# Optimization experiments

Hardware: AMD Instinct MI355X
Metric: run time of the kernel (lower is better)

## Reference

```python
import jax, jax.numpy as jnp
import numpy as np

DIM = 1024
NUM_HEADS = 16
HEAD_DIM = DIM // NUM_HEADS


def _rope_tables(seq_len, dim, dtype):
    # matches llama_rotary_embedding: inv_freq over even indices of head_dim
    inv_freq = 1.0 / (10000.0 ** (jnp.arange(0, dim, 2, dtype=jnp.float32) / dim))
    t = jnp.arange(seq_len, dtype=jnp.float32)
    freqs = jnp.outer(t, inv_freq)  # [S, dim/2]
    return jnp.cos(freqs).astype(dtype), jnp.sin(freqs).astype(dtype)


def _apply_rope(x, cos_emb, sin_emb):
    # x: [B, H, S, hd]; takes interleaved halves, concatenates rotated halves
    x1 = x[..., 0::2]
    x2 = x[..., 1::2]
    return jnp.concatenate((x1 * cos_emb - x2 * sin_emb,
                            x1 * sin_emb + x2 * cos_emb), axis=-1)


def setup_inputs() -> dict:
    key = jax.random.key(0)
    k_x, k_qkv, k_out, k_b = jax.random.split(key, 4)
    B, S, D = 2, 2048, DIM
    x = jax.random.normal(k_x, (B, S, D), dtype=jnp.float32)
    # torch nn.Linear weights are [out_features, in_features]
    w_qkv = jax.random.normal(k_qkv, (3 * D, D), dtype=jnp.float32) * (1.0 / np.sqrt(D))
    w_out = jax.random.normal(k_out, (D, D), dtype=jnp.float32) * (1.0 / np.sqrt(D))
    b_out = jax.random.normal(k_b, (D,), dtype=jnp.float32) * 0.01
    return {"x": x, "w_qkv": w_qkv, "w_out": w_out, "b_out": b_out}


def reference(x, w_qkv, w_out, b_out):
    B, S, D = x.shape
    H, hd = NUM_HEADS, HEAD_DIM
    qkv = jnp.einsum('bsd,ed->bse', x, w_qkv)  # [B, S, 3D]
    q, k, v = jnp.split(qkv, 3, axis=-1)
    # [B, S, D] -> [B, H, S, hd]
    q, k, v = (t.reshape(B, S, H, hd).transpose(0, 2, 1, 3) for t in (q, k, v))
    cos_emb, sin_emb = _rope_tables(S, hd, x.dtype)  # [S, hd/2]
    q = _apply_rope(q, cos_emb, sin_emb)
    k = _apply_rope(k, cos_emb, sin_emb)
    scores = jnp.einsum('bhqd,bhkd->bhqk', q, k) / jnp.sqrt(jnp.asarray(hd, x.dtype))
    attn = jax.nn.softmax(scores, axis=-1)
    out = jnp.einsum('bhqk,bhkd->bhqd', attn, v)
    out = out.transpose(0, 2, 1, 3).reshape(B, S, D)
    return jnp.einsum('bsd,ed->bse', out, w_out) + b_out
```

## Files before the change

### kernel.cpp

```cpp
#include <hip/hip_runtime.h>
#include <math.h>

typedef __bf16 bf16_t;
typedef bf16_t bf16x8 __attribute__((ext_vector_type(8)));
typedef bf16_t bf16x4 __attribute__((ext_vector_type(4)));
typedef short  s16x4  __attribute__((ext_vector_type(4)));
typedef float  f32x4  __attribute__((ext_vector_type(4)));

#define DIM_   1024
#define NHEADS 16
#define HDIM   64
#define SEQ    2048
#define BATCH  2

#define QK_SCALE 0.18033688011112042f

__device__ __forceinline__ s16x4 as_s16x4(bf16x4 v) {
    union { bf16x4 b; s16x4 s; } u; u.b = v; return u.s;
}

__device__ __forceinline__ void gld16(const bf16_t* g, bf16_t* l) {
    __builtin_amdgcn_global_load_lds(
        (const __attribute__((address_space(1))) void*)g,
        (__attribute__((address_space(3))) void*)l, 16, 0, 0);
}

#define XCNT   (4096u * 1024u)
#define WQCNT  (3072u * 1024u)
#define WOCNT  (1024u * 1024u)
__global__ __launch_bounds__(256) void cast3(const float* __restrict__ s0,
                                             const float* __restrict__ s1,
                                             const float* __restrict__ s2,
                                             bf16_t* __restrict__ d0,
                                             bf16_t* __restrict__ d1,
                                             bf16_t* __restrict__ d2) {
    size_t i = ((size_t)blockIdx.x * 256 + threadIdx.x) * 8;
    const float* s; bf16_t* d; size_t off;
    if (i < XCNT)               { s = s0; d = d0; off = i; }
    else if (i < XCNT + WQCNT)  { s = s1; d = d1; off = i - XCNT; }
    else                        { s = s2; d = d2; off = i - XCNT - WQCNT; }
    float4 a = *(const float4*)(s + off);
    float4 b = *(const float4*)(s + off + 4);
    bf16x8 o = { (bf16_t)a.x, (bf16_t)a.y, (bf16_t)a.z, (bf16_t)a.w,
                 (bf16_t)b.x, (bf16_t)b.y, (bf16_t)b.z, (bf16_t)b.w };
    *(bf16x8*)(d + off) = o;
}

template <bool QKV>
__global__ __launch_bounds__(256) void gemm_lds(const bf16_t* __restrict__ A,
                                                const bf16_t* __restrict__ B,
                                                const float* __restrict__ bias,
                                                void* __restrict__ Cout,
                                                bf16_t* __restrict__ vt,
                                                int M, int N, int K) {
    __shared__ __align__(16) bf16_t As[128 * 32];
    __shared__ __align__(16) bf16_t Bs[128 * 32];
    const int tid  = threadIdx.x;
    const int m0   = blockIdx.y * 128;
    const int n0   = blockIdx.x * 128;
    const int w    = tid >> 6;
    const int lane = tid & 63;
    const int m16  = lane & 15;
    const int quad = lane >> 4;
    const int wm   = (w >> 1) * 64;
    const int wn   = (w & 1) * 64;
    const int lrow = lane >> 2;
    const int lcol = (lane & 3) * 8;

    const bf16_t* pa0 = A + (size_t)(m0 + w * 16 + lrow) * K + lcol;
    const bf16_t* pb0 = B + (size_t)(n0 + w * 16 + lrow) * K + lcol;
    bf16_t* lA0 = &As[(w * 16) * 32];
    bf16_t* lA1 = &As[(64 + w * 16) * 32];
    bf16_t* lB0 = &Bs[(w * 16) * 32];
    bf16_t* lB1 = &Bs[(64 + w * 16) * 32];

    f32x4 acc[4][4] = {};

    for (int k0 = 0; k0 < K; k0 += 32) {
        __syncthreads();
        gld16(pa0 + k0, lA0);
        gld16(pa0 + (size_t)64 * K + k0, lA1);
        gld16(pb0 + k0, lB0);
        gld16(pb0 + (size_t)64 * K + k0, lB1);
        __syncthreads();

        bf16x8 af[4], bfr[4];
#pragma unroll
        for (int i = 0; i < 4; ++i)
            af[i] = *(const bf16x8*)(&As[(wm + i * 16 + m16) * 32 + quad * 8]);
#pragma unroll
        for (int j = 0; j < 4; ++j)
            bfr[j] = *(const bf16x8*)(&Bs[(wn + j * 16 + m16) * 32 + quad * 8]);
#pragma unroll
        for (int i = 0; i < 4; ++i)
#pragma unroll
            for (int j = 0; j < 4; ++j)
                acc[i][j] = __builtin_amdgcn_mfma_f32_16x16x32_bf16(af[i], bfr[j], acc[i][j], 0, 0, 0);
    }

    if (QKV && n0 >= 2 * DIM_) {
        const int b      = m0 >> 11;
        const int s_base = (m0 & (SEQ - 1)) + wm;
#pragma unroll
        for (int j = 0; j < 4; ++j) {
            const int cit = wn + j * 16 + m16;
            const int h   = ((n0 - 2 * DIM_) >> 6) + (cit >> 6);
            const int d   = cit & 63;
            bf16_t* vrow = vt + ((size_t)(b * 16 + h) * 64 + d) * SEQ + s_base;
#pragma unroll
            for (int i = 0; i < 4; ++i) {
                bf16x4 ov = { (bf16_t)acc[i][j][0], (bf16_t)acc[i][j][1],
                              (bf16_t)acc[i][j][2], (bf16_t)acc[i][j][3] };
                *(bf16x4*)(vrow + i * 16 + quad * 4) = ov;
            }
        }
    } else if (QKV) {
        bf16_t* C = (bf16_t*)Cout;
#pragma unroll
        for (int i = 0; i < 4; ++i)
#pragma unroll
            for (int j = 0; j < 4; ++j) {
                const int col = n0 + wn + j * 16 + m16;
#pragma unroll
                for (int r = 0; r < 4; ++r)
                    C[(size_t)(m0 + wm + i * 16 + quad * 4 + r) * N + col] = (bf16_t)acc[i][j][r];
            }
    } else {
        float* C = (float*)Cout;
#pragma unroll
        for (int j = 0; j < 4; ++j) {
            const int col = n0 + wn + j * 16 + m16;
            const float bv = bias[col];
#pragma unroll
            for (int i = 0; i < 4; ++i)
#pragma unroll
                for (int r = 0; r < 4; ++r)
                    C[(size_t)(m0 + wm + i * 16 + quad * 4 + r) * N + col] = acc[i][j][r] + bv;
        }
    }
}

__global__ __launch_bounds__(256) void gemm_out64(const bf16_t* __restrict__ A,
                                                  const bf16_t* __restrict__ B,
                                                  const float* __restrict__ bias,
                                                  float* __restrict__ C,
                                                  int M, int N, int K) {
    __shared__ __align__(16) bf16_t As[128 * 32];
    __shared__ __align__(16) bf16_t Bs[64 * 32];
    const int tid  = threadIdx.x;
    const int m0   = blockIdx.y * 128;
    const int n0   = blockIdx.x * 64;
    const int w    = tid >> 6;
    const int lane = tid & 63;
    const int m16  = lane & 15;
    const int quad = lane >> 4;
    const int wm   = (w >> 1) * 64;
    const int wn   = (w & 1) * 32;
    const int lrow = lane >> 2;
    const int lcol = (lane & 3) * 8;

    const bf16_t* pa0 = A + (size_t)(m0 + w * 16 + lrow) * K + lcol;
    const bf16_t* pb0 = B + (size_t)(n0 + w * 16 + lrow) * K + lcol;
    bf16_t* lA0 = &As[(w * 16) * 32];
    bf16_t* lA1 = &As[(64 + w * 16) * 32];
    bf16_t* lB0 = &Bs[(w * 16) * 32];

    f32x4 acc[4][2] = {};

    for (int k0 = 0; k0 < K; k0 += 32) {
        __syncthreads();
        gld16(pa0 + k0, lA0);
        gld16(pa0 + (size_t)64 * K + k0, lA1);
        gld16(pb0 + k0, lB0);
        __syncthreads();

        bf16x8 af[4], bfr[2];
#pragma unroll
        for (int i = 0; i < 4; ++i)
            af[i] = *(const bf16x8*)(&As[(wm + i * 16 + m16) * 32 + quad * 8]);
#pragma unroll
        for (int j = 0; j < 2; ++j)
            bfr[j] = *(const bf16x8*)(&Bs[(wn + j * 16 + m16) * 32 + quad * 8]);
#pragma unroll
        for (int i = 0; i < 4; ++i)
#pragma unroll
            for (int j = 0; j < 2; ++j)
                acc[i][j] = __builtin_amdgcn_mfma_f32_16x16x32_bf16(af[i], bfr[j], acc[i][j], 0, 0, 0);
    }

#pragma unroll
    for (int j = 0; j < 2; ++j) {
        const int col = n0 + wn + j * 16 + m16;
        const float bv = bias[col];
#pragma unroll
        for (int i = 0; i < 4; ++i)
#pragma unroll
            for (int r = 0; r < 4; ++r)
                C[(size_t)(m0 + wm + i * 16 + quad * 4 + r) * N + col] = acc[i][j][r] + bv;
    }
}

__global__ __launch_bounds__(256) void rope_bf16(bf16_t* __restrict__ qkv) {
    __shared__ float ctab[8][32];
    __shared__ float stab[8][32];
    const int tid = threadIdx.x;
    const int sl  = tid >> 5, j = tid & 31;
    const int s   = (int)((blockIdx.x * 8 + sl) & (SEQ - 1));
    const float freq = exp2f(-0.41524101186092029f * (float)j);
    float sn, cs;
    sincosf((float)s * freq, &sn, &cs);
    ctab[sl][j] = cs;
    stab[sl][j] = sn;
    __syncthreads();

    const int gid   = blockIdx.x * 256 + tid;
    const int m     = gid >> 5;
    const int rr    = gid & 31;
    const int which = rr >> 4;
    const int hh    = rr & 15;
    const float osc = (which == 0) ? QK_SCALE : 1.0f;

    bf16_t* p = qkv + (size_t)m * (3 * DIM_) + which * DIM_ + hh * HDIM;
    union { bf16_t e[64]; bf16x8 v[8]; } X, O;
#pragma unroll
    for (int i = 0; i < 8; ++i) X.v[i] = *(const bf16x8*)(p + i * 8);
#pragma unroll
    for (int t = 0; t < 32; ++t) {
        const float x1 = (float)X.e[2 * t];
        const float x2 = (float)X.e[2 * t + 1];
        const float c  = ctab[sl][t];
        const float s2 = stab[sl][t];
        O.e[t]      = (bf16_t)((x1 * c - x2 * s2) * osc);
        O.e[32 + t] = (bf16_t)((x1 * s2 + x2 * c) * osc);
    }
#pragma unroll
    for (int i = 0; i < 8; ++i) *(bf16x8*)(p + i * 8) = O.v[i];
}

__global__ __launch_bounds__(256) void attn_mfma(const bf16_t* __restrict__ qkv,
                                                 const bf16_t* __restrict__ vt,
                                                 bf16_t* __restrict__ out) {
    __shared__ __align__(16) char smem[37888];
    bf16_t* Ks0  = (bf16_t*)smem;
    bf16_t* Vt0  = (bf16_t*)(smem + 9216);
    bf16_t* Ks1  = (bf16_t*)(smem + 18432);
    bf16_t* Vt1  = (bf16_t*)(smem + 27648);
    float*  Ored = (float*)smem;
    float*  Lred = (float*)(smem + 36864);

    const int tid  = threadIdx.x;
    const int w    = tid >> 6;
    const int lane = tid & 63;
    const int m16  = lane & 15;
    const int quad = lane >> 4;
    const int bh   = blockIdx.y;
    const int b    = bh >> 4;
    const int hh   = bh & 15;
    const int q0   = blockIdx.x * 64;

    const size_t rs = 3 * DIM_;
    const bf16_t* qbase = qkv + (size_t)(b * SEQ) * rs + hh * HDIM;
    const bf16_t* kbase = qbase + DIM_;
    const bf16_t* vtg   = vt + (size_t)bh * 64 * SEQ;

    bf16x8 qf[4][2];
#pragma unroll
    for (int n = 0; n < 4; ++n)
#pragma unroll
        for (int kt = 0; kt < 2; ++kt)
            qf[n][kt] = *(const bf16x8*)(qbase + (size_t)(q0 + n * 16 + m16) * rs + kt * 32 + quad * 8);

    f32x4 o[4][4] = {};
    float lp[4] = {};

    const int srow = tid >> 3;
    const int sc8  = (tid & 7) * 8;

    bf16x8 kreg[2], vreg[2];

#pragma unroll
    for (int p = 0; p < 2; ++p) {
        const int row = srow + p * 32;
        kreg[p] = *(const bf16x8*)(kbase + (size_t)row * rs + sc8);
        vreg[p] = *(const bf16x8*)(vtg + (size_t)row * SEQ + sc8);
    }
#pragma unroll
    for (int p = 0; p < 2; ++p) {
        const int row = srow + p * 32;
        *(bf16x8*)(&Ks0[row * 72 + sc8]) = kreg[p];
        *(bf16x8*)(&Vt0[row * 72 + sc8]) = vreg[p];
    }
    __syncthreads();

    const bf16_t* kg0 = kbase + (size_t)(64 + srow) * rs + sc8;
    const bf16_t* kg1 = kg0 + (size_t)32 * rs;
    const bf16_t* vg0 = vtg + (size_t)srow * SEQ + 64 + sc8;
    const bf16_t* vg1 = vg0 + (size_t)32 * SEQ;
    const size_t kadv = (size_t)64 * rs;

#define ATTN_BODY(T, KS, VS, KSN, VSN)                                             \
    do {                                                                           \
        const int tt = (T);                                                        \
        if (tt < 31) {                                                             \
            kreg[0] = *(const bf16x8*)(kg0);                                       \
            kreg[1] = *(const bf16x8*)(kg1);                                       \
            vreg[0] = *(const bf16x8*)(vg0);                                       \
            vreg[1] = *(const bf16x8*)(vg1);                                       \
            kg0 += kadv; kg1 += kadv; vg0 += 64; vg1 += 64;                        \
        }                                                                          \
        bf16x8 ak0 = *(const bf16x8*)(&KS[(w * 16 + m16) * 72 + 0 * 32 + quad * 8]); \
        bf16x8 ak1 = *(const bf16x8*)(&KS[(w * 16 + m16) * 72 + 1 * 32 + quad * 8]); \
        bf16x4 va[4];                                                              \
        _Pragma("unroll")                                                          \
        for (int ds = 0; ds < 4; ++ds)                                             \
            va[ds] = *(const bf16x4*)(&VS[(ds * 16 + m16) * 72 + w * 16 + quad * 4]); \
        s16x4 pb[4];                                                               \
        _Pragma("unroll")                                                          \
        for (int n = 0; n < 4; ++n) {                                              \
            f32x4 c = {};                                                          \
            c = __builtin_amdgcn_mfma_f32_16x16x32_bf16(ak0, qf[n][0], c, 0, 0, 0); \
            c = __builtin_amdgcn_mfma_f32_16x16x32_bf16(ak1, qf[n][1], c, 0, 0, 0); \
            bf16x4 pv;                                                             \
            _Pragma("unroll")                                                      \
            for (int r = 0; r < 4; ++r) {                                          \
                const float pp = __builtin_amdgcn_exp2f(c[r]);                     \
                lp[n] += pp;                                                       \
                pv[r] = (bf16_t)pp;                                                \
            }                                                                      \
            pb[n] = as_s16x4(pv);                                                  \
        }                                                                          \
        __builtin_amdgcn_s_setprio(1);                                             \
        _Pragma("unroll")                                                          \
        for (int ds = 0; ds < 4; ++ds)                                             \
            _Pragma("unroll")                                                      \
            for (int n = 0; n < 4; ++n)                                            \
                o[ds][n] = __builtin_amdgcn_mfma_f32_16x16x16bf16_1k(               \
                    as_s16x4(va[ds]), pb[n], o[ds][n], 0, 0, 0);                   \
        __builtin_amdgcn_s_setprio(0);                                             \
        if (tt < 31) {                                                             \
            _Pragma("unroll")                                                      \
            for (int p = 0; p < 2; ++p) {                                          \
                const int row = srow + p * 32;                                     \
                *(bf16x8*)(&KSN[row * 72 + sc8]) = kreg[p];                        \
                *(bf16x8*)(&VSN[row * 72 + sc8]) = vreg[p];                        \
            }                                                                      \
        }                                                                          \
        __syncthreads();                                                           \
    } while (0)

    for (int t = 0; t < 32; t += 2) {
        ATTN_BODY(t,     Ks0, Vt0, Ks1, Vt1);
        ATTN_BODY(t + 1, Ks1, Vt1, Ks0, Vt0);
    }
#undef ATTN_BODY

#pragma unroll
    for (int n = 0; n < 4; ++n) {
        lp[n] += __shfl_xor(lp[n], 16);
        lp[n] += __shfl_xor(lp[n], 32);
    }
    if (quad == 0) {
#pragma unroll
        for (int n = 0; n < 4; ++n) Lred[w * 64 + n * 16 + m16] = lp[n];
    }
    __syncthreads();
    const float linv = 1.0f / (Lred[lane] + Lred[64 + lane] + Lred[128 + lane] + Lred[192 + lane]);

    const size_t obase = (size_t)(b * SEQ + q0 + lane) * DIM_ + hh * HDIM;
#pragma unroll
    for (int p = 0; p < 4; ++p) {
        __syncthreads();
#pragma unroll
        for (int n = 0; n < 4; ++n)
#pragma unroll
            for (int r = 0; r < 4; ++r)
                Ored[w * 1040 + (quad * 4 + r) * 65 + n * 16 + m16] = o[p][n][r];
        __syncthreads();
        union { bf16_t e[4]; bf16x4 v; } ob;
#pragma unroll
        for (int d = 0; d < 4; ++d) {
            const int dd = w * 4 + d;
            const float v = Ored[dd * 65 + lane] + Ored[1040 + dd * 65 + lane] +
                            Ored[2080 + dd * 65 + lane] + Ored[3120 + dd * 65 + lane];
            ob.e[d] = (bf16_t)(v * linv);
        }
        *(bf16x4*)(out + obase + p * 16 + w * 4) = ob.v;
    }
}

extern "C" void kernel_launch(void* const* d_in, const int* in_sizes, int n_in,
                              void* d_out, int out_size, void* d_ws, size_t ws_size,
                              hipStream_t stream) {
    const float* x     = (const float*)d_in[0];
    const float* w_qkv = (const float*)d_in[1];
    const float* w_out = (const float*)d_in[2];
    const float* b_out = (const float*)d_in[3];
    float* out = (float*)d_out;

    const int M = BATCH * SEQ;

    bf16_t* qkv_b  = (bf16_t*)d_ws;
    bf16_t* attn_b = qkv_b + (size_t)M * 3 * DIM_;
    bf16_t* vt_b   = attn_b + (size_t)M * DIM_;
    bf16_t* xb     = vt_b + (size_t)BATCH * NHEADS * HDIM * SEQ;
    bf16_t* wqkvb  = xb + (size_t)M * DIM_;
    bf16_t* woutb  = wqkvb + (size_t)3 * DIM_ * DIM_;

    cast3<<<(XCNT + WQCNT + WOCNT) / (256 * 8), 256, 0, stream>>>(
        x, w_qkv, w_out, xb, wqkvb, woutb);

    gemm_lds<true><<<dim3(3 * DIM_ / 128, M / 128), 256, 0, stream>>>(
        xb, wqkvb, nullptr, qkv_b, vt_b, M, 3 * DIM_, DIM_);

    rope_bf16<<<(M * 2 * NHEADS) / 256, 256, 0, stream>>>(qkv_b);

    attn_mfma<<<dim3(SEQ / 64, BATCH * NHEADS), 256, 0, stream>>>(qkv_b, vt_b, attn_b);

    gemm_out64<<<dim3(DIM_ / 64, M / 128), 256, 0, stream>>>(
        attn_b, woutb, b_out, out, M, DIM_, DIM_);
}
```

Baseline: 213.4 us.

## Double-buffer LDS tiles in both GEMM kernels to overlap loads with MFMA

Both GEMM kernels now keep two LDS buffers per operand. Each iteration issues global_load_lds for the next K-tile into the alternate buffer before running MFMAs on the current one, so the per-iteration barrier count drops from two to one. The intent is to hide global-to-LDS latency behind compute. The cost is twice the LDS footprint, which may lower occupancy. Correctness relies on the compiler inserting the right vmcnt waits before the barrier, since the async LDS writes must complete before the next iteration reads them.

```diff
diff --git a/kernel.cpp b/kernel.cpp
--- a/kernel.cpp
+++ b/kernel.cpp
@@ -53,8 +53,8 @@
                                                 void* __restrict__ Cout,
                                                 bf16_t* __restrict__ vt,
                                                 int M, int N, int K) {
-    __shared__ __align__(16) bf16_t As[128 * 32];
-    __shared__ __align__(16) bf16_t Bs[128 * 32];
+    __shared__ __align__(16) bf16_t As[2][128 * 32];
+    __shared__ __align__(16) bf16_t Bs[2][128 * 32];
     const int tid  = threadIdx.x;
     const int m0   = blockIdx.y * 128;
     const int n0   = blockIdx.x * 128;
@@ -69,33 +69,42 @@
 
     const bf16_t* pa0 = A + (size_t)(m0 + w * 16 + lrow) * K + lcol;
     const bf16_t* pb0 = B + (size_t)(n0 + w * 16 + lrow) * K + lcol;
-    bf16_t* lA0 = &As[(w * 16) * 32];
-    bf16_t* lA1 = &As[(64 + w * 16) * 32];
-    bf16_t* lB0 = &Bs[(w * 16) * 32];
-    bf16_t* lB1 = &Bs[(64 + w * 16) * 32];
+    const int sOffA0 = (w * 16) * 32;
+    const int sOffA1 = (64 + w * 16) * 32;
+
+    gld16(pa0, (bf16_t*)As + sOffA0);
+    gld16(pa0 + (size_t)64 * K, (bf16_t*)As + sOffA1);
+    gld16(pb0, (bf16_t*)Bs + sOffA0);
+    gld16(pb0 + (size_t)64 * K, (bf16_t*)Bs + sOffA1);
+    __syncthreads();
 
     f32x4 acc[4][4] = {};
+    int buf = 0;
 
     for (int k0 = 0; k0 < K; k0 += 32) {
-        __syncthreads();
-        gld16(pa0 + k0, lA0);
-        gld16(pa0 + (size_t)64 * K + k0, lA1);
-        gld16(pb0 + k0, lB0);
-        gld16(pb0 + (size_t)64 * K + k0, lB1);
-        __syncthreads();
-
+        const int nb = buf ^ 1;
+        if (k0 + 32 < K) {
+            gld16(pa0 + k0 + 32, (bf16_t*)As + nb * 4096 + sOffA0);
+            gld16(pa0 + (size_t)64 * K + k0 + 32, (bf16_t*)As + nb * 4096 + sOffA1);
+            gld16(pb0 + k0 + 32, (bf16_t*)Bs + nb * 4096 + sOffA0);
+            gld16(pb0 + (size_t)64 * K + k0 + 32, (bf16_t*)Bs + nb * 4096 + sOffA1);
+        }
+        const bf16_t* sA = (const bf16_t*)As + buf * 4096;
+        const bf16_t* sB = (const bf16_t*)Bs + buf * 4096;
         bf16x8 af[4], bfr[4];
 #pragma unroll
         for (int i = 0; i < 4; ++i)
-            af[i] = *(const bf16x8*)(&As[(wm + i * 16 + m16) * 32 + quad * 8]);
+            af[i] = *(const bf16x8*)(sA + (wm + i * 16 + m16) * 32 + quad * 8);
 #pragma unroll
         for (int j = 0; j < 4; ++j)
-            bfr[j] = *(const bf16x8*)(&Bs[(wn + j * 16 + m16) * 32 + quad * 8]);
+            bfr[j] = *(const bf16x8*)(sB + (wn + j * 16 + m16) * 32 + quad * 8);
 #pragma unroll
         for (int i = 0; i < 4; ++i)
 #pragma unroll
             for (int j = 0; j < 4; ++j)
                 acc[i][j] = __builtin_amdgcn_mfma_f32_16x16x32_bf16(af[i], bfr[j], acc[i][j], 0, 0, 0);
+        __syncthreads();
+        buf = nb;
     }
 
     if (QKV && n0 >= 2 * DIM_) {
@@ -145,8 +154,8 @@
                                                   const float* __restrict__ bias,
                                                   float* __restrict__ C,
                                                   int M, int N, int K) {
-    __shared__ __align__(16) bf16_t As[128 * 32];
-    __shared__ __align__(16) bf16_t Bs[64 * 32];
+    __shared__ __align__(16) bf16_t As[2][128 * 32];
+    __shared__ __align__(16) bf16_t Bs[2][64 * 32];
     const int tid  = threadIdx.x;
     const int m0   = blockIdx.y * 128;
     const int n0   = blockIdx.x * 64;
@@ -161,31 +170,40 @@
 
     const bf16_t* pa0 = A + (size_t)(m0 + w * 16 + lrow) * K + lcol;
     const bf16_t* pb0 = B + (size_t)(n0 + w * 16 + lrow) * K + lcol;
-    bf16_t* lA0 = &As[(w * 16) * 32];
-    bf16_t* lA1 = &As[(64 + w * 16) * 32];
-    bf16_t* lB0 = &Bs[(w * 16) * 32];
+    const int sOff0 = (w * 16) * 32;
+    const int sOff1 = (64 + w * 16) * 32;
+
+    gld16(pa0, (bf16_t*)As + sOff0);
+    gld16(pa0 + (size_t)64 * K, (bf16_t*)As + sOff1);
+    gld16(pb0, (bf16_t*)Bs + sOff0);
+    __syncthreads();
 
     f32x4 acc[4][2] = {};
+    int buf = 0;
 
     for (int k0 = 0; k0 < K; k0 += 32) {
-        __syncthreads();
-        gld16(pa0 + k0, lA0);
-        gld16(pa0 + (size_t)64 * K + k0, lA1);
-        gld16(pb0 + k0, lB0);
-        __syncthreads();
-
+        const int nb = buf ^ 1;
+        if (k0 + 32 < K) {
+            gld16(pa0 + k0 + 32, (bf16_t*)As + nb * 4096 + sOff0);
+            gld16(pa0 + (size_t)64 * K + k0 + 32, (bf16_t*)As + nb * 4096 + sOff1);
+            gld16(pb0 + k0 + 32, (bf16_t*)Bs + nb * 2048 + sOff0);
+        }
+        const bf16_t* sA = (const bf16_t*)As + buf * 4096;
+        const bf16_t* sB = (const bf16_t*)Bs + buf * 2048;
         bf16x8 af[4], bfr[2];
 #pragma unroll
         for (int i = 0; i < 4; ++i)
-            af[i] = *(const bf16x8*)(&As[(wm + i * 16 + m16) * 32 + quad * 8]);
+            af[i] = *(const bf16x8*)(sA + (wm + i * 16 + m16) * 32 + quad * 8);
 #pragma unroll
         for (int j = 0; j < 2; ++j)
-            bfr[j] = *(const bf16x8*)(&Bs[(wn + j * 16 + m16) * 32 + quad * 8]);
+            bfr[j] = *(const bf16x8*)(sB + (wn + j * 16 + m16) * 32 + quad * 8);
 #pragma unroll
         for (int i = 0; i < 4; ++i)
 #pragma unroll
             for (int j = 0; j < 2; ++j)
                 acc[i][j] = __builtin_amdgcn_mfma_f32_16x16x32_bf16(af[i], bfr[j], acc[i][j], 0, 0, 0);
+        __syncthreads();
+        buf = nb;
     }
 
 #pragma unroll
```

Measured after the change: 206.8 us. 1.03x faster.
